# Optimization experiments

Measured on AMD Instinct MI355X. Metric: run time of the kernel, lower is better.

Reference implementation:

```python
import jax, jax.numpy as jnp
import numpy as np

SPATIAL_SHAPES = [(100, 100), (50, 50), (25, 25), (13, 13)]  # (h, w) per level
D_MODEL, N_HEADS, N_LEVELS, N_POINTS = 256, 8, 4, 4
B = 2
S = sum(h * w for h, w in SPATIAL_SHAPES)  # 13294
Q = S  # encoder self-attention: num_queries == sequence_length


def setup_inputs() -> dict:
    key = jax.random.key(0)
    ks = jax.random.split(key, 12)
    d = D_MODEL
    hlp = N_HEADS * N_LEVELS * N_POINTS
    scale = 0.02
    starts = np.cumsum([0] + [h * w for h, w in SPATIAL_SHAPES[:-1]])
    return {
        "hidden_states": jax.random.normal(ks[0], (B, Q, d), jnp.float32),
        "encoder_hidden_states": jax.random.normal(ks[1], (B, S, d), jnp.float32),
        "reference_points": jax.random.uniform(ks[2], (B, Q, N_LEVELS, 2), jnp.float32),
        "W_value": jax.random.normal(ks[3], (d, d), jnp.float32) * scale,
        "b_value": jnp.zeros((d,), jnp.float32),
        "W_off": jax.random.normal(ks[4], (d, hlp * 2), jnp.float32) * scale,
        "b_off": jax.random.normal(ks[5], (hlp * 2,), jnp.float32) * scale,
        "W_attn": jax.random.normal(ks[6], (d, hlp), jnp.float32) * scale,
        "b_attn": jnp.zeros((hlp,), jnp.float32),
        "W_out": jax.random.normal(ks[7], (d, d), jnp.float32) * scale,
        "b_out": jnp.zeros((d,), jnp.float32),
        "spatial_shapes": jnp.asarray(SPATIAL_SHAPES, jnp.int32),
        "level_start_index": jnp.asarray(starts, jnp.int32),
    }


def bilinear_sample(img, grid):
    # img: [N, C, h, w]; grid: [N, Q, P, 2] xy in [-1, 1]
    # F.grid_sample(mode='bilinear', padding_mode='zeros', align_corners=False)
    N, C, h, w = img.shape
    Qg, Pg = grid.shape[1], grid.shape[2]
    x = ((grid[..., 0] + 1.0) * w - 1.0) * 0.5
    y = ((grid[..., 1] + 1.0) * h - 1.0) * 0.5
    x0 = jnp.floor(x)
    y0 = jnp.floor(y)
    x1 = x0 + 1.0
    y1 = y0 + 1.0
    wx1 = x - x0
    wx0 = 1.0 - wx1
    wy1 = y - y0
    wy0 = 1.0 - wy1
    img_flat = img.reshape(N, C, h * w)

    def gather(xi, yi):
        valid = (xi >= 0) & (xi <= w - 1) & (yi >= 0) & (yi <= h - 1)
        xi_c = jnp.clip(xi, 0, w - 1).astype(jnp.int32)
        yi_c = jnp.clip(yi, 0, h - 1).astype(jnp.int32)
        idx = (yi_c * w + xi_c).reshape(N, 1, Qg * Pg)
        vals = jnp.take_along_axis(img_flat, idx, axis=2)  # [N, C, Q*P]
        return vals * valid.reshape(N, 1, Qg * Pg).astype(img.dtype)

    out = (
        gather(x0, y0) * (wx0 * wy0).reshape(N, 1, -1)
        + gather(x1, y0) * (wx1 * wy0).reshape(N, 1, -1)
        + gather(x0, y1) * (wx0 * wy1).reshape(N, 1, -1)
        + gather(x1, y1) * (wx1 * wy1).reshape(N, 1, -1)
    )
    return out.reshape(N, C, Qg, Pg)


def reference(hidden_states, encoder_hidden_states, reference_points,
              W_value, b_value, W_off, b_off, W_attn, b_attn, W_out, b_out,
              spatial_shapes, level_start_index):
    Bq, Qn, d = hidden_states.shape
    H, L, P = N_HEADS, N_LEVELS, N_POINTS
    Dh = d // H
    value = (encoder_hidden_states @ W_value + b_value).reshape(Bq, -1, H, Dh)
    off = (hidden_states @ W_off + b_off).reshape(Bq, Qn, H, L, P, 2)
    aw = (hidden_states @ W_attn + b_attn).reshape(Bq, Qn, H, L * P)
    aw = jax.nn.softmax(aw, axis=-1).reshape(Bq, Qn, H, L, P)
    # offset normalizer is (width, height) per level
    norm = jnp.stack([spatial_shapes[:, 1], spatial_shapes[:, 0]], -1).astype(off.dtype)
    loc = reference_points[:, :, None, :, None, :] + off / norm[None, None, None, :, None, :]
    grids = 2.0 * loc - 1.0  # [B, Q, H, L, P, 2]

    starts = np.cumsum([0] + [h * w for h, w in SPATIAL_SHAPES])
    sampled = []
    for lvl, (h, w) in enumerate(SPATIAL_SHAPES):
        v = value[:, starts[lvl]:starts[lvl + 1]]              # [B, h*w, H, Dh]
        v = v.transpose(0, 2, 3, 1).reshape(Bq * H, Dh, h, w)   # [B*H, Dh, h, w]
        g = grids[:, :, :, lvl].transpose(0, 2, 1, 3, 4).reshape(Bq * H, Qn, P, 2)
        sampled.append(bilinear_sample(v, g))                   # [B*H, Dh, Q, P]
    samp = jnp.stack(sampled, axis=-2).reshape(Bq * H, Dh, Qn, L * P)
    wts = aw.transpose(0, 2, 1, 3, 4).reshape(Bq * H, 1, Qn, L * P)
    out = (samp * wts).sum(-1)                                  # [B*H, Dh, Q]
    out = out.reshape(Bq, H * Dh, Qn).transpose(0, 2, 1)        # [B, Q, d]
    out = out @ W_out + b_out
    return out, aw
```

## Files before the change

### kernel.cpp

```cpp
#include <hip/hip_runtime.h>
#include <hip/hip_bf16.h>
#include <math.h>

#define BQn 2
#define QN 13294
#define SN 13294
#define NH 8
#define DH 32
#define DM 256

typedef __attribute__((ext_vector_type(8))) short short8;
typedef __attribute__((ext_vector_type(4))) float f32x4;

__device__ __forceinline__ unsigned short f2bf(float x) {
    union { float f; unsigned int u; } c; c.f = x;
    unsigned int r = c.u + 0x7fff + ((c.u >> 16) & 1);
    return (unsigned short)(r >> 16);
}
__device__ __forceinline__ float asf(unsigned int u) {
    union { unsigned int i; float f; } c; c.i = u; return c.f;
}

__global__ __launch_bounds__(256) void conv_weights(
    const float* __restrict__ Wv, const float* __restrict__ Woff,
    const float* __restrict__ Wa, const float* __restrict__ Wout,
    unsigned short* __restrict__ WvT, unsigned short* __restrict__ WoffT,
    unsigned short* __restrict__ WaT, unsigned short* __restrict__ WoutT)
{
    const int t = blockIdx.x * 256 + threadIdx.x;
    if (t < 65536) {
        const int n = t & 255, k = t >> 8;
        WvT[(size_t)n * 256 + k] = f2bf(Wv[(size_t)k * 256 + n]);
    } else if (t < 131072) {
        const int i = t - 65536, n = i & 255, k = i >> 8;
        WoffT[(size_t)n * 256 + k] = f2bf(Woff[(size_t)k * 256 + n]);
    } else if (t < 163840) {
        const int i = t - 131072, n = i & 127, k = i >> 7;
        WaT[(size_t)n * 256 + k] = f2bf(Wa[(size_t)k * 128 + n]);
    } else if (t < 229376) {
        const int i = t - 163840, n = i & 255, k = i >> 8;
        WoutT[(size_t)n * 256 + k] = f2bf(Wout[(size_t)k * 256 + n]);
    }
}

__global__ __launch_bounds__(256) void gemm_dual(
    const float* __restrict__ A0, const float* __restrict__ A1,
    const unsigned short* __restrict__ WT0,
    const unsigned short* __restrict__ WT1,
    const float* __restrict__ bv, const float* __restrict__ boff,
    const float* __restrict__ ba,
    unsigned short* __restrict__ C0, float* __restrict__ C1, int M)
{
    __shared__ unsigned short As[64][72];
    __shared__ unsigned short Bs[128][72];
    const int tid  = threadIdx.x;
    const int lane = tid & 63, wid = tid >> 6;
    const int wr = wid >> 1, wc = wid & 1;
    const bool second = (blockIdx.x >= 2);
    const float* A = second ? A1 : A0;
    const unsigned short* WT = second ? WT1 : WT0;
    const int n0 = (second ? (int)blockIdx.x - 2 : (int)blockIdx.x) * 128;
    const int r0 = blockIdx.y * 64;

    f32x4 acc[2][4] = {};

    for (int k0 = 0; k0 < 256; k0 += 64) {
        #pragma unroll
        for (int i = 0; i < 2; ++i) {
            const int idx = i * 256 + tid;
            const int row = idx >> 3, ch = (idx & 7) << 3;
            int grow = r0 + row; if (grow >= M) grow = M - 1;
            const float4 v0 = *(const float4*)(A + (size_t)grow * 256 + k0 + ch);
            const float4 v1 = *(const float4*)(A + (size_t)grow * 256 + k0 + ch + 4);
            union { __hip_bfloat162 b[4]; uint4 u; } pk;
            pk.b[0] = __float22bfloat162_rn(make_float2(v0.x, v0.y));
            pk.b[1] = __float22bfloat162_rn(make_float2(v0.z, v0.w));
            pk.b[2] = __float22bfloat162_rn(make_float2(v1.x, v1.y));
            pk.b[3] = __float22bfloat162_rn(make_float2(v1.z, v1.w));
            *(uint4*)&As[row][ch] = pk.u;
        }
        #pragma unroll
        for (int i = 0; i < 4; ++i) {
            const int idx = i * 256 + tid;
            const int row = idx >> 3, ch = (idx & 7) << 3;
            *(uint4*)&Bs[row][ch] =
                *(const uint4*)(WT + (size_t)(n0 + row) * 256 + k0 + ch);
        }
        __syncthreads();
        #pragma unroll
        for (int kk = 0; kk < 2; ++kk) {
            const int kb = kk * 32 + (lane >> 4) * 8;
            short8 bfr[4];
            #pragma unroll
            for (int n = 0; n < 4; ++n)
                bfr[n] = *(const short8*)&Bs[wc * 64 + n * 16 + (lane & 15)][kb];
            #pragma unroll
            for (int m = 0; m < 2; ++m) {
                const short8 afr =
                    *(const short8*)&As[wr * 32 + m * 16 + (lane & 15)][kb];
                #pragma unroll
                for (int n = 0; n < 4; ++n)
                    acc[m][n] = __builtin_amdgcn_mfma_f32_16x16x32_bf16(
                        afr, bfr[n], acc[m][n], 0, 0, 0);
            }
        }
        __syncthreads();
    }

    #pragma unroll
    for (int m = 0; m < 2; ++m)
        #pragma unroll
        for (int n = 0; n < 4; ++n) {
            const int col = n0 + wc * 64 + n * 16 + (lane & 15);
            const float bsv = second
                ? ((col < 256) ? boff[col] : ba[col - 256])
                : bv[col];
            #pragma unroll
            for (int j = 0; j < 4; ++j) {
                const int row = r0 + wr * 32 + m * 16 + (lane >> 4) * 4 + j;
                if (row >= M) continue;
                const float v = acc[m][n][j] + bsv;
                if (second) {
                    C1[(size_t)row * 384 + col] = v;
                } else {
                    const int b = (row >= SN), s = row - b * SN;
                    const int h = col >> 5, dh = col & 31;
                    C0[(((size_t)b * NH + h) * SN + s) * DH + dh] = f2bf(v);
                }
            }
        }
}

__global__ __launch_bounds__(256) void gemm_out(
    const unsigned short* __restrict__ A,
    const unsigned short* __restrict__ WT,
    const float* __restrict__ bias,
    float* __restrict__ C, int M)
{
    __shared__ unsigned short As[64][72];
    __shared__ unsigned short Bs[128][72];
    const int tid  = threadIdx.x;
    const int lane = tid & 63, wid = tid >> 6;
    const int wr = wid >> 1, wc = wid & 1;
    const int r0 = blockIdx.y * 64, n0 = blockIdx.x * 128;

    f32x4 acc[2][4] = {};

    for (int k0 = 0; k0 < 256; k0 += 64) {
        #pragma unroll
        for (int i = 0; i < 2; ++i) {
            const int idx = i * 256 + tid;
            const int row = idx >> 3, ch = (idx & 7) << 3;
            int grow = r0 + row; if (grow >= M) grow = M - 1;
            *(uint4*)&As[row][ch] =
                *(const uint4*)(A + (size_t)grow * 256 + k0 + ch);
        }
        #pragma unroll
        for (int i = 0; i < 4; ++i) {
            const int idx = i * 256 + tid;
            const int row = idx >> 3, ch = (idx & 7) << 3;
            *(uint4*)&Bs[row][ch] =
                *(const uint4*)(WT + (size_t)(n0 + row) * 256 + k0 + ch);
        }
        __syncthreads();
        #pragma unroll
        for (int kk = 0; kk < 2; ++kk) {
            const int kb = kk * 32 + (lane >> 4) * 8;
            short8 bfr[4];
            #pragma unroll
            for (int n = 0; n < 4; ++n)
                bfr[n] = *(const short8*)&Bs[wc * 64 + n * 16 + (lane & 15)][kb];
            #pragma unroll
            for (int m = 0; m < 2; ++m) {
                const short8 afr =
                    *(const short8*)&As[wr * 32 + m * 16 + (lane & 15)][kb];
                #pragma unroll
                for (int n = 0; n < 4; ++n)
                    acc[m][n] = __builtin_amdgcn_mfma_f32_16x16x32_bf16(
                        afr, bfr[n], acc[m][n], 0, 0, 0);
            }
        }
        __syncthreads();
    }

    #pragma unroll
    for (int m = 0; m < 2; ++m)
        #pragma unroll
        for (int n = 0; n < 4; ++n) {
            const int col = n0 + wc * 64 + n * 16 + (lane & 15);
            const float bsv = bias[col];
            #pragma unroll
            for (int j = 0; j < 4; ++j) {
                const int row = r0 + wr * 32 + m * 16 + (lane >> 4) * 4 + j;
                if (row >= M) continue;
                C[(size_t)row * 256 + col] = acc[m][n][j] + bsv;
            }
        }
}

__global__ __launch_bounds__(256) void ms_sample(
    const unsigned short* __restrict__ value,
    const float* __restrict__ offaw,
    const float* __restrict__ refp,
    unsigned short* __restrict__ outh,
    float* __restrict__ awout)
{
    const int h  = blockIdx.x & 7;
    const int qc = blockIdx.x >> 3;
    const int lc = threadIdx.x & 7;
    const int bq = qc * 32 + (threadIdx.x >> 3);
    if (bq >= BQn * QN) return;
    const int b  = (bq >= QN);
    const int gbase = threadIdx.x & 56;

    const float* rowp = offaw + (size_t)bq * 384;

    const float2 lw2 = *(const float2*)(rowp + 256 + h * 16 + lc * 2);
    float m = fmaxf(lw2.x, lw2.y);
    #pragma unroll
    for (int d = 1; d < 8; d <<= 1) m = fmaxf(m, __shfl_xor(m, d, 8));
    float e0 = __expf(lw2.x - m), e1 = __expf(lw2.y - m);
    float s = e0 + e1;
    #pragma unroll
    for (int d = 1; d < 8; d <<= 1) s += __shfl_xor(s, d, 8);
    const float inv = 1.f / s;
    e0 *= inv; e1 *= inv;
    *(float2*)(awout + (size_t)bq * 128 + h * 16 + lc * 2) = make_float2(e0, e1);

    const int lvl = lc >> 1;
    const int wi  = (lvl == 0) ? 100 : (lvl == 1) ? 50 : (lvl == 2) ? 25 : 13;
    const float fw = (float)wi;
    const int sti = (lvl == 0) ? 0 : (lvl == 1) ? 10000 : (lvl == 2) ? 12500 : 13125;
    const float rw = (lvl == 0) ? 0.01f : (lvl == 1) ? 0.02f
                   : (lvl == 2) ? 0.04f : (1.0f / 13.0f);
    const float2 rp = *(const float2*)(refp + (size_t)bq * 8 + lvl * 2);
    const float4 o4 = *(const float4*)(rowp + h * 32 + lc * 4);

    int   rA0, rB0, cA0, cB0, rA1, rB1, cA1, cB1;
    float wxA0, wxB0, wyA0, wyB0, wxA1, wxB1, wyA1, wyB1;

    auto prep = [&](float ox, float oy, float ek,
                    int& rA, int& rB, int& cA, int& cB,
                    float& wxA, float& wxB, float& wyA, float& wyB) {
        const float x = fmaf(fmaf(ox, rw, rp.x), fw, -0.5f);
        const float y = fmaf(fmaf(oy, rw, rp.y), fw, -0.5f);
        const float x0f = floorf(x), y0f = floorf(y);
        const int ix = (int)x0f, iy = (int)y0f;
        const float wx1 = x - x0f, wy1 = y - y0f;
        wxA = ((unsigned)ix        < (unsigned)wi) ? 1.f - wx1 : 0.f;
        wxB = ((unsigned)(ix + 1)  < (unsigned)wi) ? wx1       : 0.f;
        wyA = (((unsigned)iy       < (unsigned)wi) ? 1.f - wy1 : 0.f) * ek;
        wyB = (((unsigned)(iy + 1) < (unsigned)wi) ? wy1       : 0.f) * ek;
        const int xc0 = min(max(ix, 0),     wi - 1);
        const int xc1 = min(max(ix + 1, 0), wi - 1);
        const int yc0 = min(max(iy, 0),     wi - 1);
        const int yc1 = min(max(iy + 1, 0), wi - 1);
        rA = sti + yc0 * wi; rB = sti + yc1 * wi;
        cA = xc0;            cB = xc1;
    };
    prep(o4.x, o4.y, e0, rA0, rB0, cA0, cB0, wxA0, wxB0, wyA0, wyB0);
    prep(o4.z, o4.w, e1, rA1, rB1, cA1, cB1, wxA1, wxB1, wyA1, wyB1);

    const char* hplane = (const char*)(value + (size_t)h * SN * DH);
    const unsigned lnoff = (unsigned)b * (NH * SN * DH * 2) + lc * 8;

    float ax = 0.f, ay = 0.f, az = 0.f, aw_ = 0.f;

    #pragma unroll
    for (int p = 0; p < 16; ++p) {
        const int src = gbase + (p >> 1);
        const int   rA  = __shfl((p & 1) ? rA1  : rA0,  src, 64);
        const int   rB  = __shfl((p & 1) ? rB1  : rB0,  src, 64);
        const int   cA  = __shfl((p & 1) ? cA1  : cA0,  src, 64);
        const int   cB  = __shfl((p & 1) ? cB1  : cB0,  src, 64);
        const float wxA = __shfl((p & 1) ? wxA1 : wxA0, src, 64);
        const float wxB = __shfl((p & 1) ? wxB1 : wxB0, src, 64);
        const float wyA = __shfl((p & 1) ? wyA1 : wyA0, src, 64);
        const float wyB = __shfl((p & 1) ? wyB1 : wyB0, src, 64);

        #pragma unroll
        for (int c = 0; c < 4; ++c) {
            const int cell  = ((c >> 1) ? rB : rA) + ((c & 1) ? cB : cA);
            const float cw  = ((c & 1) ? wxB : wxA) * ((c >> 1) ? wyB : wyA);
            const uint2 v = *(const uint2*)(hplane + ((unsigned)cell * 64u + lnoff));
            ax  = fmaf(cw, asf(v.x << 16),          ax);
            ay  = fmaf(cw, asf(v.x & 0xffff0000u),  ay);
            az  = fmaf(cw, asf(v.y << 16),          az);
            aw_ = fmaf(cw, asf(v.y & 0xffff0000u),  aw_);
        }
    }

    ushort4 o;
    o.x = f2bf(ax); o.y = f2bf(ay); o.z = f2bf(az); o.w = f2bf(aw_);
    *(ushort4*)(outh + (size_t)bq * 256 + h * 32 + lc * 4) = o;
}

extern "C" void kernel_launch(void* const* d_in, const int* in_sizes, int n_in,
                              void* d_out, int out_size, void* d_ws, size_t ws_size,
                              hipStream_t stream) {
    const float* hs   = (const float*)d_in[0];
    const float* enc  = (const float*)d_in[1];
    const float* refp = (const float*)d_in[2];
    const float* Wv   = (const float*)d_in[3];
    const float* bv   = (const float*)d_in[4];
    const float* Woff = (const float*)d_in[5];
    const float* boff = (const float*)d_in[6];
    const float* Wa   = (const float*)d_in[7];
    const float* ba   = (const float*)d_in[8];
    const float* Wout = (const float*)d_in[9];
    const float* bout = (const float*)d_in[10];

    float* out    = (float*)d_out;
    float* aw_out = out + (size_t)BQn * QN * 256;

    const size_t MQ = (size_t)BQn * QN;
    unsigned short* valueb = (unsigned short*)d_ws;
    float* offaw = (float*)(valueb + MQ * 256);
    unsigned short* outh  = (unsigned short*)(offaw + MQ * 384);
    unsigned short* WvT   = outh + MQ * 256;
    unsigned short* WcatT = WvT + 256 * 256;
    unsigned short* WoutT = WcatT + 384 * 256;

    const int M = (int)MQ;
    const dim3 blk(256);

    conv_weights<<<896, blk, 0, stream>>>(Wv, Woff, Wa, Wout,
                                          WvT, WcatT, WcatT + 65536, WoutT);

    const int my = (M + 63) / 64;
    gemm_dual<<<dim3(5, my), blk, 0, stream>>>(
        enc, hs, WvT, WcatT, bv, boff, ba, valueb, offaw, M);

    const int qchunks = (M + 31) / 32;
    ms_sample<<<8 * qchunks, blk, 0, stream>>>(valueb, offaw, refp,
                                               outh, aw_out);

    gemm_out<<<dim3(2, my), blk, 0, stream>>>(outh, WoutT, bout, out, M);
}
```

Measured before the change: 128.8 us.

## Split sampling points across two half-groups per query, doubling threads per query

The ms_sample kernel now assigns 16 lanes per (query, head) instead of 8. Each lane handles one sampling point's prep and one softmax logit, and the two halves each accumulate 8 points over the same channel slice. A cross-lane xor-shuffle then combines the halves before writing. This halves the serial gather loop per thread and the number of points each lane prepares, which should expose more memory-level parallelism. In exchange it doubles the grid, adds a reduction shuffle, and leaves half the lanes idle during the store.

```diff
diff --git a/kernel.cpp b/kernel.cpp
--- a/kernel.cpp
+++ b/kernel.cpp
@@ -207,59 +207,55 @@
 {
     const int h  = blockIdx.x & 7;
     const int qc = blockIdx.x >> 3;
-    const int lc = threadIdx.x & 7;
-    const int bq = qc * 32 + (threadIdx.x >> 3);
+    const int gl = threadIdx.x & 15;
+    const int bq = qc * 16 + (threadIdx.x >> 4);
     if (bq >= BQn * QN) return;
     const int b  = (bq >= QN);
-    const int gbase = threadIdx.x & 56;
+    const int lc = gl & 7;
+    const int ph = gl >> 3;
+    const int gbase = threadIdx.x & 48;
 
     const float* rowp = offaw + (size_t)bq * 384;
 
-    const float2 lw2 = *(const float2*)(rowp + 256 + h * 16 + lc * 2);
-    float m = fmaxf(lw2.x, lw2.y);
-    #pragma unroll
-    for (int d = 1; d < 8; d <<= 1) m = fmaxf(m, __shfl_xor(m, d, 8));
-    float e0 = __expf(lw2.x - m), e1 = __expf(lw2.y - m);
-    float s = e0 + e1;
-    #pragma unroll
-    for (int d = 1; d < 8; d <<= 1) s += __shfl_xor(s, d, 8);
-    const float inv = 1.f / s;
-    e0 *= inv; e1 *= inv;
-    *(float2*)(awout + (size_t)bq * 128 + h * 16 + lc * 2) = make_float2(e0, e1);
-
-    const int lvl = lc >> 1;
+    const float lg = rowp[256 + h * 16 + gl];
+    float mx = lg;
+    #pragma unroll
+    for (int d = 1; d < 16; d <<= 1) mx = fmaxf(mx, __shfl_xor(mx, d, 16));
+    float e = __expf(lg - mx);
+    float s = e;
+    #pragma unroll
+    for (int d = 1; d < 16; d <<= 1) s += __shfl_xor(s, d, 16);
+    e *= 1.f / s;
+    awout[(size_t)bq * 128 + h * 16 + gl] = e;
+
+    const int lvl = gl >> 2;
     const int wi  = (lvl == 0) ? 100 : (lvl == 1) ? 50 : (lvl == 2) ? 25 : 13;
     const float fw = (float)wi;
     const int sti = (lvl == 0) ? 0 : (lvl == 1) ? 10000 : (lvl == 2) ? 12500 : 13125;
     const float rw = (lvl == 0) ? 0.01f : (lvl == 1) ? 0.02f
                    : (lvl == 2) ? 0.04f : (1.0f / 13.0f);
     const float2 rp = *(const float2*)(refp + (size_t)bq * 8 + lvl * 2);
-    const float4 o4 = *(const float4*)(rowp + h * 32 + lc * 4);
-
-    int   rA0, rB0, cA0, cB0, rA1, rB1, cA1, cB1;
-    float wxA0, wxB0, wyA0, wyB0, wxA1, wxB1, wyA1, wyB1;
-
-    auto prep = [&](float ox, float oy, float ek,
-                    int& rA, int& rB, int& cA, int& cB,
-                    float& wxA, float& wxB, float& wyA, float& wyB) {
-        const float x = fmaf(fmaf(ox, rw, rp.x), fw, -0.5f);
-        const float y = fmaf(fmaf(oy, rw, rp.y), fw, -0.5f);
+    const float2 o2 = *(const float2*)(rowp + h * 32 + gl * 2);
+
+    int rA, rB, cA, cB;
+    float wxA, wxB, wyA, wyB;
+    {
+        const float x = fmaf(fmaf(o2.x, rw, rp.x), fw, -0.5f);
+        const float y = fmaf(fmaf(o2.y, rw, rp.y), fw, -0.5f);
         const float x0f = floorf(x), y0f = floorf(y);
         const int ix = (int)x0f, iy = (int)y0f;
         const float wx1 = x - x0f, wy1 = y - y0f;
         wxA = ((unsigned)ix        < (unsigned)wi) ? 1.f - wx1 : 0.f;
         wxB = ((unsigned)(ix + 1)  < (unsigned)wi) ? wx1       : 0.f;
-        wyA = (((unsigned)iy       < (unsigned)wi) ? 1.f - wy1 : 0.f) * ek;
-        wyB = (((unsigned)(iy + 1) < (unsigned)wi) ? wy1       : 0.f) * ek;
+        wyA = (((unsigned)iy       < (unsigned)wi) ? 1.f - wy1 : 0.f) * e;
+        wyB = (((unsigned)(iy + 1) < (unsigned)wi) ? wy1       : 0.f) * e;
         const int xc0 = min(max(ix, 0),     wi - 1);
         const int xc1 = min(max(ix + 1, 0), wi - 1);
         const int yc0 = min(max(iy, 0),     wi - 1);
         const int yc1 = min(max(iy + 1, 0), wi - 1);
         rA = sti + yc0 * wi; rB = sti + yc1 * wi;
         cA = xc0;            cB = xc1;
-    };
-    prep(o4.x, o4.y, e0, rA0, rB0, cA0, cB0, wxA0, wxB0, wyA0, wyB0);
-    prep(o4.z, o4.w, e1, rA1, rB1, cA1, cB1, wxA1, wxB1, wyA1, wyB1);
+    }
 
     const char* hplane = (const char*)(value + (size_t)h * SN * DH);
     const unsigned lnoff = (unsigned)b * (NH * SN * DH * 2) + lc * 8;
@@ -267,21 +263,21 @@
     float ax = 0.f, ay = 0.f, az = 0.f, aw_ = 0.f;
 
     #pragma unroll
-    for (int p = 0; p < 16; ++p) {
-        const int src = gbase + (p >> 1);
-        const int   rA  = __shfl((p & 1) ? rA1  : rA0,  src, 64);
-        const int   rB  = __shfl((p & 1) ? rB1  : rB0,  src, 64);
-        const int   cA  = __shfl((p & 1) ? cA1  : cA0,  src, 64);
-        const int   cB  = __shfl((p & 1) ? cB1  : cB0,  src, 64);
-        const float wxA = __shfl((p & 1) ? wxA1 : wxA0, src, 64);
-        const float wxB = __shfl((p & 1) ? wxB1 : wxB0, src, 64);
-        const float wyA = __shfl((p & 1) ? wyA1 : wyA0, src, 64);
-        const float wyB = __shfl((p & 1) ? wyB1 : wyB0, src, 64);
+    for (int pp = 0; pp < 8; ++pp) {
+        const int src = gbase + ph * 8 + pp;
+        const int   rAs = __shfl(rA,  src, 64);
+        const int   rBs = __shfl(rB,  src, 64);
+        const int   cAs = __shfl(cA,  src, 64);
+        const int   cBs = __shfl(cB,  src, 64);
+        const float xAs = __shfl(wxA, src, 64);
+        const float xBs = __shfl(wxB, src, 64);
+        const float yAs = __shfl(wyA, src, 64);
+        const float yBs = __shfl(wyB, src, 64);
 
         #pragma unroll
         for (int c = 0; c < 4; ++c) {
-            const int cell  = ((c >> 1) ? rB : rA) + ((c & 1) ? cB : cA);
-            const float cw  = ((c & 1) ? wxB : wxA) * ((c >> 1) ? wyB : wyA);
+            const int cell  = ((c >> 1) ? rBs : rAs) + ((c & 1) ? cBs : cAs);
+            const float cw  = ((c & 1) ? xBs : xAs) * ((c >> 1) ? yBs : yAs);
             const uint2 v = *(const uint2*)(hplane + ((unsigned)cell * 64u + lnoff));
             ax  = fmaf(cw, asf(v.x << 16),          ax);
             ay  = fmaf(cw, asf(v.x & 0xffff0000u),  ay);
@@ -290,9 +286,16 @@
         }
     }
 
-    ushort4 o;
-    o.x = f2bf(ax); o.y = f2bf(ay); o.z = f2bf(az); o.w = f2bf(aw_);
-    *(ushort4*)(outh + (size_t)bq * 256 + h * 32 + lc * 4) = o;
+    ax  += __shfl_xor(ax,  8, 64);
+    ay  += __shfl_xor(ay,  8, 64);
+    az  += __shfl_xor(az,  8, 64);
+    aw_ += __shfl_xor(aw_, 8, 64);
+
+    if (ph == 0) {
+        ushort4 o;
+        o.x = f2bf(ax); o.y = f2bf(ay); o.z = f2bf(az); o.w = f2bf(aw_);
+        *(ushort4*)(outh + (size_t)bq * 256 + h * 32 + lc * 4) = o;
+    }
 }
 
 extern "C" void kernel_launch(void* const* d_in, const int* in_sizes, int n_in,
@@ -331,7 +334,7 @@
     gemm_dual<<<dim3(5, my), blk, 0, stream>>>(
         enc, hs, WvT, WcatT, bv, boff, ba, valueb, offaw, M);
 
-    const int qchunks = (M + 31) / 32;
+    const int qchunks = (M + 15) / 16;
     ms_sample<<<8 * qchunks, blk, 0, stream>>>(valueb, offaw, refp,
                                                outh, aw_out);
 
```

Result: no change. 129.1 us (+0.2%).
